# Kernel tuning notes

Hardware: AMD Instinct MI355X
Metric: run time of the kernel (lower is better)

The kernel has to match this reference:

```python
import jax, jax.numpy as jnp
import numpy as np

LN_EPS = 1e-5
NUM_HEADS = 16

def _layernorm(x, g, b):
    mu = jnp.mean(x, axis=-1, keepdims=True)
    var = jnp.mean(jnp.square(x - mu), axis=-1, keepdims=True)
    return (x - mu) * jax.lax.rsqrt(var + LN_EPS) * g + b

def setup_inputs() -> dict:
    key = jax.random.key(0)
    ks = jax.random.split(key, 8)
    B, N, C, Hf = 8, 4096, 1024, 2048
    s = 1.0 / np.sqrt(C)
    return {
        "x": jax.random.normal(ks[0], (B, N, C), jnp.float32),
        "ln1_g": jnp.ones((C,), jnp.float32),
        "ln1_b": jnp.zeros((C,), jnp.float32),
        "ln2_g": jnp.ones((C,), jnp.float32),
        "ln2_b": jnp.zeros((C,), jnp.float32),
        "wq": jax.random.normal(ks[1], (C, C), jnp.float32) * s,
        "wk": jax.random.normal(ks[2], (C, C), jnp.float32) * s,
        "wv": jax.random.normal(ks[3], (C, C), jnp.float32) * s,
        "proj_w": jax.random.normal(ks[4], (C, C), jnp.float32) * s,
        "proj_b": jnp.zeros((C,), jnp.float32),
        "fc1_w": jax.random.normal(ks[5], (C, Hf), jnp.float32) * s,
        "fc1_b": jnp.zeros((Hf,), jnp.float32),
        "fc2_w": jax.random.normal(ks[6], (Hf, C), jnp.float32) / np.sqrt(Hf),
        "fc2_b": jnp.zeros((C,), jnp.float32),
    }

def reference(x, ln1_g, ln1_b, ln2_g, ln2_b, wq, wk, wv, proj_w, proj_b,
              fc1_w, fc1_b, fc2_w, fc2_b):
    B, N, C = x.shape
    H = NUM_HEADS
    d = C // H
    scale = d ** -0.5

    # --- attention branch (note: attention over the head_dim axis, d x d scores) ---
    h = _layernorm(x, ln1_g, ln1_b)
    def split(t):  # (B,N,C) -> (B,H,d,N), matching permute(0,2,3,1)
        return jnp.transpose(t.reshape(B, N, H, d), (0, 2, 3, 1))
    q = split(h @ wq)
    k = split(h @ wk)
    v = split(h @ wv)
    attn = jax.nn.softmax(jnp.einsum("bhdn,bhen->bhde", q, k) * scale, axis=-1)  # (B,H,d,d)
    o = jnp.einsum("bhde,bhen->bhdn", attn, v)           # (B,H,d,N)
    o = jnp.transpose(o, (0, 2, 1, 3)).reshape(B, N, C)  # transpose(1,2).reshape
    x = x + (o @ proj_w + proj_b)

    # --- MLP branch ---
    h2 = _layernorm(x, ln2_g, ln2_b)
    h2 = jax.nn.gelu(h2 @ fc1_w + fc1_b, approximate=False)
    x = x + (h2 @ fc2_w + fc2_b)
    return x
```

## Files before the change

### kernel.cpp

```cpp
#include <hip/hip_runtime.h>
#include <cmath>

typedef __attribute__((ext_vector_type(8))) _Float16 f16x8;
typedef __attribute__((ext_vector_type(8))) unsigned short u16x8;
typedef __attribute__((ext_vector_type(4))) float f32x4;

__device__ __forceinline__ unsigned short f2h(float f) {
  return __builtin_bit_cast(unsigned short, (_Float16)f);
}

__device__ __forceinline__ void async16(const void* gp, void* lp) {
  __builtin_amdgcn_global_load_lds(
      (const __attribute__((address_space(1))) void*)gp,
      (__attribute__((address_space(3))) void*)lp, 16, 0, 0);
}

__global__ __launch_bounds__(256) void transpose_cast(
    const float* __restrict__ W, unsigned short* __restrict__ WT, int K, int N) {
  __shared__ float tile[32][33];
  const int tx = threadIdx.x & 31, ty = threadIdx.x >> 5;
  const int n0 = blockIdx.x * 32, k0 = blockIdx.y * 32;
#pragma unroll
  for (int r = 0; r < 4; ++r)
    tile[ty + 8 * r][tx] = W[(size_t)(k0 + ty + 8 * r) * N + n0 + tx];
  __syncthreads();
#pragma unroll
  for (int r = 0; r < 4; ++r)
    WT[(size_t)(n0 + ty + 8 * r) * K + k0 + tx] = f2h(tile[tx][ty + 8 * r]);
}

__global__ __launch_bounds__(256) void layernorm_cast(
    const float* __restrict__ x, const float* __restrict__ g,
    const float* __restrict__ bt, unsigned short* __restrict__ out) {
  const int row = blockIdx.x, tid = threadIdx.x;
  const float4 v = ((const float4*)(x + (size_t)row * 1024))[tid];
  float s = v.x + v.y + v.z + v.w;
  float ss = v.x * v.x + v.y * v.y + v.z * v.z + v.w * v.w;
#pragma unroll
  for (int off = 32; off >= 1; off >>= 1) {
    s += __shfl_down(s, off);
    ss += __shfl_down(ss, off);
  }
  __shared__ float red[10];
  const int wave = tid >> 6, lane = tid & 63;
  if (lane == 0) { red[wave] = s; red[4 + wave] = ss; }
  __syncthreads();
  if (tid == 0) {
    float S = red[0] + red[1] + red[2] + red[3];
    float SS = red[4] + red[5] + red[6] + red[7];
    float mu = S * (1.f / 1024.f);
    float var = SS * (1.f / 1024.f) - mu * mu;
    red[8] = mu;
    red[9] = rsqrtf(var + 1e-5f);
  }
  __syncthreads();
  const float mu = red[8], rs = red[9];
  const float4 gv = ((const float4*)g)[tid];
  const float4 bv = ((const float4*)bt)[tid];
  ushort4 r;
  r.x = f2h((v.x - mu) * rs * gv.x + bv.x);
  r.y = f2h((v.y - mu) * rs * gv.y + bv.y);
  r.z = f2h((v.z - mu) * rs * gv.z + bv.z);
  r.w = f2h((v.w - mu) * rs * gv.w + bv.w);
  ((ushort4*)(out + (size_t)row * 1024))[tid] = r;
}

__global__ __launch_bounds__(256) void gemm_bt(
    const unsigned short* __restrict__ A, const unsigned short* __restrict__ BT,
    int M, int N, int K,
    const float* __restrict__ bias, const float* __restrict__ resid,
    float* __restrict__ outF, unsigned short* __restrict__ outB, int mode) {
  __shared__ unsigned short sA[2 * 128 * 32];
  __shared__ unsigned short sB[2 * 128 * 32];
  const int tid = threadIdx.x, wave = tid >> 6, lane = tid & 63;
  const int l16 = lane & 15, g16 = lane >> 4;
  const int wm = wave & 1, wn = wave >> 1;

  const int lin = blockIdx.y * gridDim.x + blockIdx.x;
  const int t_ = lin >> 3;
  const int bx = t_ % gridDim.x;
  const int by = (lin & 7) + 8 * (t_ / gridDim.x);
  const int row0 = by * 128, col0 = bx * 128;

  const int r_ = tid >> 2;
  const int s_ = ((tid & 3) ^ ((tid >> 3) & 3)) * 8;
  const unsigned short* pA = A + (size_t)(row0 + r_) * K + s_;
  const unsigned short* pB = BT + (size_t)(col0 + r_) * K + s_;
  unsigned short* dA = sA + wave * 512;
  unsigned short* dB = sB + wave * 512;
  const size_t rstep = (size_t)64 * K;

  f32x4 acc[4][4] = {};

  for (int k0 = 0; k0 < K; k0 += 64) {
    __syncthreads();
    async16(pA, dA);
    async16(pA + rstep, dA + 2048);
    async16(pA + 32, dA + 4096);
    async16(pA + rstep + 32, dA + 6144);
    async16(pB, dB);
    async16(pB + rstep, dB + 2048);
    async16(pB + 32, dB + 4096);
    async16(pB + rstep + 32, dB + 6144);
    pA += 64;
    pB += 64;
    __syncthreads();
#pragma unroll
    for (int kk = 0; kk < 2; ++kk) {
      f16x8 af[4], bf[4];
#pragma unroll
      for (int i = 0; i < 4; ++i) {
        const int ra = wm * 64 + i * 16 + l16;
        af[i] = __builtin_bit_cast(f16x8,
            *(const u16x8*)&sA[kk * 4096 + ra * 32 + (g16 ^ ((ra >> 1) & 3)) * 8]);
      }
#pragma unroll
      for (int j = 0; j < 4; ++j) {
        const int rb = wn * 64 + j * 16 + l16;
        bf[j] = __builtin_bit_cast(f16x8,
            *(const u16x8*)&sB[kk * 4096 + rb * 32 + (g16 ^ ((rb >> 1) & 3)) * 8]);
      }
#pragma unroll
      for (int i = 0; i < 4; ++i)
#pragma unroll
        for (int j = 0; j < 4; ++j)
          acc[i][j] = __builtin_amdgcn_mfma_f32_16x16x32_f16(af[i], bf[j], acc[i][j], 0, 0, 0);
    }
  }

#pragma unroll
  for (int i = 0; i < 4; ++i) {
#pragma unroll
    for (int j = 0; j < 4; ++j) {
      const int col = col0 + wn * 64 + j * 16 + l16;
      const float bcol = (mode != 0) ? bias[col] : 0.f;
#pragma unroll
      for (int r = 0; r < 4; ++r) {
        const int row = row0 + wm * 64 + i * 16 + g16 * 4 + r;
        const size_t idx = (size_t)row * N + col;
        const float val = acc[i][j][r];
        if (mode == 1) {
          outF[idx] = val + bcol + resid[idx];
        } else if (mode == 2) {
          const float t = val + bcol;
          outB[idx] = f2h(0.5f * t * (1.0f + erff(t * 0.70710678118f)));
        } else {
          outB[idx] = f2h(val);
        }
      }
    }
  }
}

__global__ __launch_bounds__(256) void attn_qk_part(
    const unsigned short* __restrict__ qkv, float* __restrict__ sp) {
  constexpr int ST = 72;
  __shared__ unsigned short sQT[64 * ST];
  __shared__ unsigned short sKT[64 * ST];
  const int bx = blockIdx.x, bh = bx >> 2, chunk = bx & 3;
  const int b = bh >> 4, h = bh & 15;
  const size_t base = (size_t)b * 4096 * 3072 + (size_t)h * 64;
  const int tid = threadIdx.x, wave = tid >> 6, lane = tid & 63;
  const int l16 = lane & 15, g16 = lane >> 4;
  const int wm = wave & 1, wn = wave >> 1;
  const int srow = tid >> 2, sseg = tid & 3;

  f32x4 acc[2][2] = {};

  for (int ntl = 0; ntl < 16; ++ntl) {
    const int nt = chunk * 16 + ntl;
    __syncthreads();
    const size_t roff = base + (size_t)(nt * 64 + srow) * 3072 + sseg * 16;
    const u16x8 q0 = *(const u16x8*)(qkv + roff);
    const u16x8 q1 = *(const u16x8*)(qkv + roff + 8);
    const u16x8 k0 = *(const u16x8*)(qkv + roff + 1024);
    const u16x8 k1 = *(const u16x8*)(qkv + roff + 1032);
#pragma unroll
    for (int ii = 0; ii < 8; ++ii) {
      sQT[(sseg * 16 + ii) * ST + srow] = q0[ii];
      sQT[(sseg * 16 + 8 + ii) * ST + srow] = q1[ii];
      sKT[(sseg * 16 + ii) * ST + srow] = k0[ii];
      sKT[(sseg * 16 + 8 + ii) * ST + srow] = k1[ii];
    }
    __syncthreads();
#pragma unroll
    for (int kk = 0; kk < 2; ++kk) {
      f16x8 aq[2], bk[2];
#pragma unroll
      for (int i = 0; i < 2; ++i)
        aq[i] = __builtin_bit_cast(f16x8,
            *(const u16x8*)&sQT[(wm * 32 + i * 16 + l16) * ST + kk * 32 + g16 * 8]);
#pragma unroll
      for (int j = 0; j < 2; ++j)
        bk[j] = __builtin_bit_cast(f16x8,
            *(const u16x8*)&sKT[(wn * 32 + j * 16 + l16) * ST + kk * 32 + g16 * 8]);
#pragma unroll
      for (int i = 0; i < 2; ++i)
#pragma unroll
        for (int j = 0; j < 2; ++j)
          acc[i][j] = __builtin_amdgcn_mfma_f32_16x16x32_f16(aq[i], bk[j], acc[i][j], 0, 0, 0);
    }
  }

  float* o = sp + (size_t)bx * 4096;
#pragma unroll
  for (int i = 0; i < 2; ++i)
#pragma unroll
    for (int j = 0; j < 2; ++j)
#pragma unroll
      for (int r = 0; r < 4; ++r)
        o[(wm * 32 + i * 16 + g16 * 4 + r) * 64 + (wn * 32 + j * 16 + l16)] = acc[i][j][r];
}

__global__ __launch_bounds__(64) void attn_softmax(
    const float* __restrict__ sp, unsigned short* __restrict__ am) {
  const int bh = blockIdx.x, dd = threadIdx.x;
  const float* p = sp + (size_t)bh * 4 * 4096 + dd * 64;
  float row[64];
#pragma unroll
  for (int e4 = 0; e4 < 16; ++e4) {
    const float4 a = ((const float4*)p)[e4];
    const float4 b_ = ((const float4*)(p + 4096))[e4];
    const float4 c_ = ((const float4*)(p + 8192))[e4];
    const float4 d_ = ((const float4*)(p + 12288))[e4];
    row[4 * e4 + 0] = a.x + b_.x + c_.x + d_.x;
    row[4 * e4 + 1] = a.y + b_.y + c_.y + d_.y;
    row[4 * e4 + 2] = a.z + b_.z + c_.z + d_.z;
    row[4 * e4 + 3] = a.w + b_.w + c_.w + d_.w;
  }
  float mx = -1e30f;
#pragma unroll
  for (int e = 0; e < 64; ++e) mx = fmaxf(mx, row[e]);
  float sum = 0.f;
#pragma unroll
  for (int e = 0; e < 64; ++e) {
    row[e] = __expf(0.125f * (row[e] - mx));
    sum += row[e];
  }
  const float inv = 1.0f / sum;
  unsigned short* q = am + (size_t)bh * 4096 + dd * 64;
#pragma unroll
  for (int e = 0; e < 64; ++e) q[e] = f2h(row[e] * inv);
}

__global__ __launch_bounds__(256) void attn_pv(
    const unsigned short* __restrict__ qkv, const unsigned short* __restrict__ am,
    unsigned short* __restrict__ o) {
  const int bx = blockIdx.x, bh = bx >> 2, chunk = bx & 3;
  const int b = bh >> 4, h = bh & 15;
  const size_t base = (size_t)b * 4096 * 3072 + (size_t)h * 64;
  const int tid = threadIdx.x, wave = tid >> 6, lane = tid & 63;
  const int l16 = lane & 15, g16 = lane >> 4;
  const int wm = wave & 1, wn = wave >> 1;

  f16x8 amf[2][2];
#pragma unroll
  for (int i = 0; i < 2; ++i)
#pragma unroll
    for (int kk = 0; kk < 2; ++kk)
      amf[i][kk] = __builtin_bit_cast(f16x8,
          *(const u16x8*)(am + (size_t)bh * 4096 +
                          (wm * 32 + i * 16 + l16) * 64 + kk * 32 + g16 * 8));

  for (int ntl = 0; ntl < 16; ++ntl) {
    const int nt = chunk * 16 + ntl;
    f32x4 oc[2][2] = {};
#pragma unroll
    for (int kk = 0; kk < 2; ++kk) {
#pragma unroll
      for (int j = 0; j < 2; ++j) {
        const f16x8 vf = __builtin_bit_cast(f16x8,
            *(const u16x8*)(qkv + base + 2048 +
                            (size_t)(nt * 64 + wn * 32 + j * 16 + l16) * 3072 +
                            kk * 32 + g16 * 8));
#pragma unroll
        for (int i = 0; i < 2; ++i)
          oc[i][j] = __builtin_amdgcn_mfma_f32_16x16x32_f16(amf[i][kk], vf, oc[i][j], 0, 0, 0);
      }
    }
#pragma unroll
    for (int i = 0; i < 2; ++i)
#pragma unroll
      for (int j = 0; j < 2; ++j)
#pragma unroll
        for (int r = 0; r < 4; ++r) {
          const int dd = wm * 32 + i * 16 + g16 * 4 + r;
          const int nf = nt * 64 + wn * 32 + j * 16 + l16;
          const int row = b * 4096 + dd * 64 + h * 4 + (nf >> 10);
          o[(size_t)row * 1024 + (nf & 1023)] = f2h(oc[i][j][r]);
        }
  }
}

extern "C" void kernel_launch(void* const* d_in, const int* in_sizes, int n_in,
                              void* d_out, int out_size, void* d_ws, size_t ws_size,
                              hipStream_t stream) {
  (void)in_sizes; (void)n_in; (void)out_size; (void)ws_size;
  const float* x = (const float*)d_in[0];
  const float* ln1g = (const float*)d_in[1];
  const float* ln1b = (const float*)d_in[2];
  const float* ln2g = (const float*)d_in[3];
  const float* ln2b = (const float*)d_in[4];
  const float* wq = (const float*)d_in[5];
  const float* wk = (const float*)d_in[6];
  const float* wv = (const float*)d_in[7];
  const float* projw = (const float*)d_in[8];
  const float* projb = (const float*)d_in[9];
  const float* fc1w = (const float*)d_in[10];
  const float* fc1b = (const float*)d_in[11];
  const float* fc2w = (const float*)d_in[12];
  const float* fc2b = (const float*)d_in[13];
  float* out = (float*)d_out;

  const int M = 8 * 4096, C = 1024, HF = 2048;

  unsigned short* p = (unsigned short*)d_ws;
  unsigned short* wqkvT = p; p += (size_t)3 * C * C;
  unsigned short* prT = p; p += (size_t)C * C;
  unsigned short* f1T = p; p += (size_t)HF * C;
  unsigned short* f2T = p; p += (size_t)C * HF;
  unsigned short* hb = p;  p += (size_t)M * C;
  unsigned short* qkvb = p; p += (size_t)M * 3 * C;
  unsigned short* ob = hb;
  unsigned short* h2 = qkvb;
  unsigned short* h3 = qkvb + (size_t)M * C;
  float* Spart = (float*)hb;
  unsigned short* Am = wqkvT;

  transpose_cast<<<dim3(C / 32, C / 32), 256, 0, stream>>>(wq, wqkvT, C, C);
  transpose_cast<<<dim3(C / 32, C / 32), 256, 0, stream>>>(wk, wqkvT + (size_t)C * C, C, C);
  transpose_cast<<<dim3(C / 32, C / 32), 256, 0, stream>>>(wv, wqkvT + (size_t)2 * C * C, C, C);
  transpose_cast<<<dim3(C / 32, C / 32), 256, 0, stream>>>(projw, prT, C, C);
  transpose_cast<<<dim3(HF / 32, C / 32), 256, 0, stream>>>(fc1w, f1T, C, HF);
  transpose_cast<<<dim3(C / 32, HF / 32), 256, 0, stream>>>(fc2w, f2T, HF, C);

  layernorm_cast<<<M, 256, 0, stream>>>(x, ln1g, ln1b, hb);

  gemm_bt<<<dim3(3 * C / 128, M / 128), 256, 0, stream>>>(
      hb, wqkvT, M, 3 * C, C, nullptr, nullptr, nullptr, qkvb, 0);

  attn_qk_part<<<512, 256, 0, stream>>>(qkvb, Spart);
  attn_softmax<<<128, 64, 0, stream>>>(Spart, Am);
  attn_pv<<<512, 256, 0, stream>>>(qkvb, Am, ob);

  const dim3 g1(C / 128, M / 128);
  gemm_bt<<<g1, 256, 0, stream>>>(ob, prT, M, C, C, projb, x, out, nullptr, 1);

  layernorm_cast<<<M, 256, 0, stream>>>(out, ln2g, ln2b, h2);

  gemm_bt<<<dim3(HF / 128, M / 128), 256, 0, stream>>>(h2, f1T, M, HF, C, fc1b, nullptr, nullptr, h3, 2);
  gemm_bt<<<g1, 256, 0, stream>>>(h3, f2T, M, C, HF, fc2b, out, out, nullptr, 1);
}
```

Baseline: 1.361 ms.

## Stage GEMM epilogue through LDS for vectorized fp16 stores; split residual into separate kernels

The GEMM epilogue now writes each wave's tile into shared memory and then stores 16-byte vectors of fp16 to global memory, replacing strided scalar stores. The residual add moves out of the GEMM: the proj and fc2 GEMMs emit fp16, and new kernels add bias and residual in fp32. The first of these also fuses the second layernorm. This aims at better write coalescing and a lighter epilogue. In exchange it adds an extra pass over fp16 intermediates, and rounding the proj and fc2 outputs to fp16 before the residual add loses precision.

```diff
diff --git a/kernel.cpp b/kernel.cpp
--- a/kernel.cpp
+++ b/kernel.cpp
@@ -7,6 +7,9 @@
 
 __device__ __forceinline__ unsigned short f2h(float f) {
   return __builtin_bit_cast(unsigned short, (_Float16)f);
+}
+__device__ __forceinline__ float h2f(unsigned short u) {
+  return (float)__builtin_bit_cast(_Float16, u);
 }
 
 __device__ __forceinline__ void async16(const void* gp, void* lp) {
@@ -65,13 +68,75 @@
   ((ushort4*)(out + (size_t)row * 1024))[tid] = r;
 }
 
+__global__ __launch_bounds__(256) void resid_ln(
+    const float* __restrict__ x, const unsigned short* __restrict__ pr,
+    const float* __restrict__ pb, const float* __restrict__ g,
+    const float* __restrict__ bt, float* __restrict__ out,
+    unsigned short* __restrict__ h2) {
+  const int row = blockIdx.x, tid = threadIdx.x;
+  const size_t off = (size_t)row * 1024;
+  const float4 xv = ((const float4*)(x + off))[tid];
+  const ushort4 pv = ((const ushort4*)(pr + off))[tid];
+  const float4 bb = ((const float4*)pb)[tid];
+  float4 v;
+  v.x = xv.x + h2f(pv.x) + bb.x;
+  v.y = xv.y + h2f(pv.y) + bb.y;
+  v.z = xv.z + h2f(pv.z) + bb.z;
+  v.w = xv.w + h2f(pv.w) + bb.w;
+  ((float4*)(out + off))[tid] = v;
+  float s = v.x + v.y + v.z + v.w;
+  float ss = v.x * v.x + v.y * v.y + v.z * v.z + v.w * v.w;
+#pragma unroll
+  for (int o = 32; o >= 1; o >>= 1) {
+    s += __shfl_down(s, o);
+    ss += __shfl_down(ss, o);
+  }
+  __shared__ float red[10];
+  const int wave = tid >> 6, lane = tid & 63;
+  if (lane == 0) { red[wave] = s; red[4 + wave] = ss; }
+  __syncthreads();
+  if (tid == 0) {
+    float S = red[0] + red[1] + red[2] + red[3];
+    float SS = red[4] + red[5] + red[6] + red[7];
+    float mu = S * (1.f / 1024.f);
+    float var = SS * (1.f / 1024.f) - mu * mu;
+    red[8] = mu;
+    red[9] = rsqrtf(var + 1e-5f);
+  }
+  __syncthreads();
+  const float mu = red[8], rs = red[9];
+  const float4 gv = ((const float4*)g)[tid];
+  const float4 bv = ((const float4*)bt)[tid];
+  ushort4 r;
+  r.x = f2h((v.x - mu) * rs * gv.x + bv.x);
+  r.y = f2h((v.y - mu) * rs * gv.y + bv.y);
+  r.z = f2h((v.z - mu) * rs * gv.z + bv.z);
+  r.w = f2h((v.w - mu) * rs * gv.w + bv.w);
+  ((ushort4*)(h2 + off))[tid] = r;
+}
+
+__global__ __launch_bounds__(256) void resid_add(
+    float* __restrict__ out, const unsigned short* __restrict__ y,
+    const float* __restrict__ b) {
+  const int row = blockIdx.x, tid = threadIdx.x;
+  const size_t off = (size_t)row * 1024;
+  float4 o = ((const float4*)(out + off))[tid];
+  const ushort4 yv = ((const ushort4*)(y + off))[tid];
+  const float4 bv = ((const float4*)b)[tid];
+  o.x += h2f(yv.x) + bv.x;
+  o.y += h2f(yv.y) + bv.y;
+  o.z += h2f(yv.z) + bv.z;
+  o.w += h2f(yv.w) + bv.w;
+  ((float4*)(out + off))[tid] = o;
+}
+
 __global__ __launch_bounds__(256) void gemm_bt(
     const unsigned short* __restrict__ A, const unsigned short* __restrict__ BT,
     int M, int N, int K,
-    const float* __restrict__ bias, const float* __restrict__ resid,
-    float* __restrict__ outF, unsigned short* __restrict__ outB, int mode) {
-  __shared__ unsigned short sA[2 * 128 * 32];
-  __shared__ unsigned short sB[2 * 128 * 32];
+    const float* __restrict__ bias, unsigned short* __restrict__ outB, int gelu) {
+  __shared__ unsigned short smem[17408];
+  unsigned short* sA = smem;
+  unsigned short* sB = smem + 8192;
   const int tid = threadIdx.x, wave = tid >> 6, lane = tid & 63;
   const int l16 = lane & 15, g16 = lane >> 4;
   const int wm = wave & 1, wn = wave >> 1;
@@ -128,27 +193,26 @@
     }
   }
 
-#pragma unroll
-  for (int i = 0; i < 4; ++i) {
-#pragma unroll
-    for (int j = 0; j < 4; ++j) {
-      const int col = col0 + wn * 64 + j * 16 + l16;
-      const float bcol = (mode != 0) ? bias[col] : 0.f;
+  __syncthreads();
+  unsigned short* scr = smem + wave * 4352;
+#pragma unroll
+  for (int j = 0; j < 4; ++j) {
+    const float bcol = gelu ? bias[col0 + wn * 64 + j * 16 + l16] : 0.f;
+#pragma unroll
+    for (int i = 0; i < 4; ++i)
 #pragma unroll
       for (int r = 0; r < 4; ++r) {
-        const int row = row0 + wm * 64 + i * 16 + g16 * 4 + r;
-        const size_t idx = (size_t)row * N + col;
-        const float val = acc[i][j][r];
-        if (mode == 1) {
-          outF[idx] = val + bcol + resid[idx];
-        } else if (mode == 2) {
-          const float t = val + bcol;
-          outB[idx] = f2h(0.5f * t * (1.0f + erff(t * 0.70710678118f)));
-        } else {
-          outB[idx] = f2h(val);
-        }
+        float val = acc[i][j][r] + bcol;
+        if (gelu) val = 0.5f * val * (1.0f + erff(val * 0.70710678118f));
+        scr[(i * 16 + g16 * 4 + r) * 68 + j * 16 + l16] = f2h(val);
       }
-    }
+  }
+#pragma unroll
+  for (int rr = 0; rr < 8; ++rr) {
+    const int lr = rr * 8 + (lane >> 3);
+    const int lc = (lane & 7) * 8;
+    const u16x8 val = *(const u16x8*)&scr[lr * 68 + lc];
+    *(u16x8*)(outB + (size_t)(row0 + wm * 64 + lr) * N + col0 + wn * 64 + lc) = val;
   }
 }
 
@@ -313,19 +377,22 @@
   float* out = (float*)d_out;
 
   const int M = 8 * 4096, C = 1024, HF = 2048;
+  const size_t MC = (size_t)M * C;
 
   unsigned short* p = (unsigned short*)d_ws;
   unsigned short* wqkvT = p; p += (size_t)3 * C * C;
   unsigned short* prT = p; p += (size_t)C * C;
   unsigned short* f1T = p; p += (size_t)HF * C;
   unsigned short* f2T = p; p += (size_t)C * HF;
-  unsigned short* hb = p;  p += (size_t)M * C;
-  unsigned short* qkvb = p; p += (size_t)M * 3 * C;
-  unsigned short* ob = hb;
-  unsigned short* h2 = qkvb;
-  unsigned short* h3 = qkvb + (size_t)M * C;
+  unsigned short* hb = p;  p += MC;
+  unsigned short* qkvb = p; p += 3 * MC;
   float* Spart = (float*)hb;
   unsigned short* Am = wqkvT;
+  unsigned short* ob = hb;
+  unsigned short* projout = qkvb;
+  unsigned short* h2 = qkvb + 2 * MC;
+  unsigned short* h3 = qkvb;
+  unsigned short* yb = hb;
 
   transpose_cast<<<dim3(C / 32, C / 32), 256, 0, stream>>>(wq, wqkvT, C, C);
   transpose_cast<<<dim3(C / 32, C / 32), 256, 0, stream>>>(wk, wqkvT + (size_t)C * C, C, C);
@@ -337,17 +404,22 @@
   layernorm_cast<<<M, 256, 0, stream>>>(x, ln1g, ln1b, hb);
 
   gemm_bt<<<dim3(3 * C / 128, M / 128), 256, 0, stream>>>(
-      hb, wqkvT, M, 3 * C, C, nullptr, nullptr, nullptr, qkvb, 0);
+      hb, wqkvT, M, 3 * C, C, nullptr, qkvb, 0);
 
   attn_qk_part<<<512, 256, 0, stream>>>(qkvb, Spart);
   attn_softmax<<<128, 64, 0, stream>>>(Spart, Am);
   attn_pv<<<512, 256, 0, stream>>>(qkvb, Am, ob);
 
-  const dim3 g1(C / 128, M / 128);
-  gemm_bt<<<g1, 256, 0, stream>>>(ob, prT, M, C, C, projb, x, out, nullptr, 1);
-
-  layernorm_cast<<<M, 256, 0, stream>>>(out, ln2g, ln2b, h2);
-
-  gemm_bt<<<dim3(HF / 128, M / 128), 256, 0, stream>>>(h2, f1T, M, HF, C, fc1b, nullptr, nullptr, h3, 2);
-  gemm_bt<<<g1, 256, 0, stream>>>(h3, f2T, M, C, HF, fc2b, out, out, nullptr, 1);
-}
+  gemm_bt<<<dim3(C / 128, M / 128), 256, 0, stream>>>(
+      ob, prT, M, C, C, nullptr, projout, 0);
+
+  resid_ln<<<M, 256, 0, stream>>>(x, projout, projb, ln2g, ln2b, out, h2);
+
+  gemm_bt<<<dim3(HF / 128, M / 128), 256, 0, stream>>>(
+      h2, f1T, M, HF, C, fc1b, h3, 1);
+
+  gemm_bt<<<dim3(C / 128, M / 128), 256, 0, stream>>>(
+      h3, f2T, M, C, HF, nullptr, yb, 0);
+
+  resid_add<<<M, 256, 0, stream>>>(out, yb, fc2b);
+}
```

After: 1.140 ms. 1.19x faster.
